# Kernel tuning notes

Hardware: AMD Instinct MI355X
Metric: run time of the kernel (lower is better)

Reference implementation:

```python
import jax, jax.numpy as jnp
import numpy as np

B, T, A, H, E = 512, 64, 32, 512, 32


def sinusoidal_pos_encoding(t, dim):
    # t: (B, T) float positions -> (B, T, dim)
    half = dim // 2
    freqs = jnp.exp(-jnp.log(10000.0) * jnp.arange(half, dtype=jnp.float32) / half)
    ang = t[..., None] * freqs  # (B, T, half)
    return jnp.concatenate([jnp.sin(ang), jnp.cos(ang)], axis=-1)


def cat_linear(x, W, b, cat_ids):
    # x: (B, T, Din); W: (E, Din, Dout); b: (E, Dout); cat_ids: (B,)
    Wg = W[cat_ids]            # (B, Din, Dout) gathered per-sample weights
    bg = b[cat_ids][:, None]   # (B, 1, Dout)
    return jnp.einsum('btd,bdh->bth', x, Wg) + bg


def swish(x):
    return x * jax.nn.sigmoid(x)


def setup_inputs() -> dict:
    key = jax.random.key(0)
    ks = jax.random.split(key, 10)
    s = lambda fan_in: 1.0 / np.sqrt(fan_in)
    return {
        'actions': jax.random.normal(ks[0], (B, T, A), dtype=jnp.float32),
        'timesteps': jax.random.uniform(ks[1], (B,), dtype=jnp.float32),
        'cat_ids': jax.random.randint(ks[2], (B,), 0, E),
        'W1': jax.random.normal(ks[3], (E, A, H), dtype=jnp.float32) * s(A),
        'b1': jnp.zeros((E, H), dtype=jnp.float32),
        'W2': jax.random.normal(ks[4], (E, 2 * H, H), dtype=jnp.float32) * s(2 * H),
        'b2': jnp.zeros((E, H), dtype=jnp.float32),
        'W3': jax.random.normal(ks[5], (E, H, H), dtype=jnp.float32) * s(H),
        'b3': jnp.zeros((E, H), dtype=jnp.float32),
    }


def reference(actions, timesteps, cat_ids, W1, b1, W2, b2, W3, b3):
    b, t, _ = actions.shape
    timesteps_bt = jnp.broadcast_to(timesteps[:, None], (b, t))
    a_emb = cat_linear(actions, W1, b1, cat_ids)              # (B, T, H)
    tau_emb = sinusoidal_pos_encoding(timesteps_bt, H).astype(a_emb.dtype)
    x = jnp.concatenate([a_emb, tau_emb], axis=-1)            # (B, T, 2H)
    x = swish(cat_linear(x, W2, b2, cat_ids))                 # (B, T, H)
    x = cat_linear(x, W3, b3, cat_ids)                        # (B, T, H)
    return x
```

## Files before the change

### kernel.cpp

```cpp
#include <hip/hip_runtime.h>
#include <hip/hip_bf16.h>

#define B_ 512
#define T_ 64
#define A_ 32
#define H_ 512
#define E_ 32
#define MAX_TASKS 272
#define CAP_ 168
#define GRID_ (8 * CAP_)

typedef unsigned short u16;
typedef unsigned int u32;
typedef __attribute__((ext_vector_type(8))) short short8;
typedef __attribute__((ext_vector_type(4))) float floatx4;

static __device__ __forceinline__ u16 f2bf(float f) {
    u32 u = __builtin_bit_cast(u32, f);
    u += 0x7fffu + ((u >> 16) & 1u);
    return (u16)(u >> 16);
}

static __device__ __forceinline__ void gl2lds16(const u16* g, u16* l) {
    __builtin_amdgcn_global_load_lds(
        (const __attribute__((address_space(1))) void*)g,
        (__attribute__((address_space(3))) void*)l, 16, 0, 0);
}

__global__ void group_kernel(const int* __restrict__ cat_ids,
                             int* __restrict__ sample_list,
                             int4* __restrict__ tasks,
                             int* __restrict__ itemlist) {
    __shared__ int cnt[E_], off[E_], cur[E_], toff[E_], jc[8];
    __shared__ int total, fb;
    int tid = threadIdx.x;
    if (tid < E_) { cnt[tid] = 0; cur[tid] = 0; }
    __syncthreads();
    int e = cat_ids[tid];
    atomicAdd(&cnt[e], 1);
    __syncthreads();
    if (tid == 0) {
        int run = 0, trun = 0;
        for (int i = 0; i < E_; i++) {
            off[i] = run;  run += cnt[i];
            toff[i] = trun; trun += (cnt[i] + 1) >> 1;
        }
        total = trun;
    }
    __syncthreads();
    if (tid < E_) {
        int c = cnt[tid], o = off[tid], to = toff[tid];
        for (int j = 0; j < c; j += 2)
            tasks[to++] = make_int4(tid, o + j, (c - j >= 2) ? 2 : 1, 0);
    }
    if (tid < 8) {
        int J = 0;
        for (int cc = 0; cc < 4; cc++) J += 4 * ((cnt[tid + 8 * cc] + 1) >> 1);
        jc[tid] = J;
    }
    __syncthreads();
    if (tid == 0) {
        int f = 0;
        for (int x = 0; x < 8; x++) if (jc[x] > CAP_) f = 1;
        fb = f;
    }
    __syncthreads();
    if (!fb) {
        if (tid < 8) {
            int j = 0;
            for (int cc = 0; cc < 4; cc++) {
                int ee = tid + 8 * cc;
                int nt = (cnt[ee] + 1) >> 1, t0 = toff[ee];
                for (int t = t0; t < t0 + nt; t++)
                    for (int nb = 0; nb < 4; nb++) {
                        itemlist[tid + 8 * j] = (t << 2) | nb;
                        j++;
                    }
            }
            for (; j < CAP_; j++) itemlist[tid + 8 * j] = -1;
        }
    } else {
        for (int f = tid; f < GRID_; f += 512)
            itemlist[f] = (f < 4 * total) ? f : -1;
    }
    int p = atomicAdd(&cur[e], 1);
    sample_list[off[e] + p] = tid;
}

__global__ __launch_bounds__(256) void embed_kernel(
        const float* __restrict__ actions, const float* __restrict__ timesteps,
        const int* __restrict__ cat_ids, const float* __restrict__ W1,
        const float* __restrict__ b1, u16* __restrict__ a_emb,
        u16* __restrict__ tau_emb) {
    int b = blockIdx.x;
    int tid = threadIdx.x;
    int e = cat_ids[b];
    float tval = timesteps[b];

    {
        float freq = expf(-9.210340371976184f * (float)tid * (1.0f / 256.0f));
        float ang = tval * freq;
        tau_emb[b * H_ + tid]       = f2bf(sinf(ang));
        tau_emb[b * H_ + 256 + tid] = f2bf(cosf(ang));
    }

    __shared__ float act[T_ * A_];
    const float* asrc = actions + (size_t)b * T_ * A_;
    for (int i = tid; i < T_ * A_; i += 256) act[i] = asrc[i];
    __syncthreads();

    const float* w1 = W1 + (size_t)e * A_ * H_;
    int n0 = tid, n1 = tid + 256;
    float wA[A_], wB[A_];
#pragma unroll
    for (int k = 0; k < A_; k++) {
        wA[k] = w1[k * H_ + n0];
        wB[k] = w1[k * H_ + n1];
    }
    float bA = b1[e * H_ + n0], bB = b1[e * H_ + n1];
    u16* orow = a_emb + (size_t)b * T_ * H_;
    for (int tt = 0; tt < T_; tt++) {
        float accA = bA, accB = bB;
#pragma unroll
        for (int k = 0; k < A_; k++) {
            float a = act[tt * A_ + k];
            accA = fmaf(a, wA[k], accA);
            accB = fmaf(a, wB[k], accB);
        }
        orow[tt * H_ + n0] = f2bf(accA);
        orow[tt * H_ + n1] = f2bf(accB);
    }
}

__global__ __launch_bounds__(256) void convert_transpose(
        const float* __restrict__ W, u16* __restrict__ Wt, int K) {
    int n = blockIdx.y * 256 + threadIdx.x;
    int k0 = blockIdx.x * 32;
    int e = blockIdx.z;
    const float* src = W + ((size_t)e * K + k0) * H_ + n;
    short8 out[4];
#pragma unroll
    for (int j = 0; j < 32; j++)
        out[j >> 3][j & 7] = (short)f2bf(src[(size_t)j * H_]);
    u16* dst = Wt + ((size_t)e * H_ + n) * K + k0;
#pragma unroll
    for (int c = 0; c < 4; c++) *(short8*)(dst + c * 8) = out[c];
}

template <int DIN, bool HAS_TAU, bool DO_SWISH, bool OUT_BF16>
__global__ __launch_bounds__(256, 4) void moe_gemm(
        const u16* __restrict__ xsrc, const u16* __restrict__ tau,
        const u16* __restrict__ Wt, const float* __restrict__ bias,
        const int* __restrict__ sample_list, const int4* __restrict__ tasks,
        const int* __restrict__ itemlist, void* __restrict__ outp) {
    int item = itemlist[blockIdx.x];
    if (item < 0) return;
    int4 task = tasks[item >> 2];
    int nb = item & 3;
    int ns = task.z;
    int e = task.x;
    int s0 = sample_list[task.y];
    int s1 = (ns > 1) ? sample_list[task.y + 1] : s0;
    int n0 = nb * 128;

    int tid = threadIdx.x;
    int lane = tid & 63, wv = tid >> 6;
    int wr = wv >> 1, wc = wv & 1;
    int quad = lane >> 4, c15 = lane & 15;
    int r8 = lane >> 3, cg = lane & 7;

    __shared__ __align__(16) u16 xs[128 * 64];
    __shared__ __align__(16) u16 wt[128 * 64];

    floatx4 acc[4][4];
    floatx4 zero4 = {0.f, 0.f, 0.f, 0.f};
#pragma unroll
    for (int i = 0; i < 4; i++)
#pragma unroll
        for (int j = 0; j < 4; j++) acc[i][j] = zero4;

    const u16* wbase = Wt + (size_t)(e * H_ + n0) * DIN;
    int kc_sw = (cg ^ r8) * 8;

    for (int k0 = 0; k0 < DIN; k0 += 64) {
        bool use_tau = HAS_TAU && (k0 >= 512);
#pragma unroll
        for (int h = 0; h < 4; h++) {
            int rbase = h * 32 + wv * 8;
            int row = rbase + r8;
            int s = (rbase < 64) ? s0 : s1;
            int t = row & 63;
            const u16* g = use_tau
                ? (tau + (size_t)s * H_ + (k0 - 512) + kc_sw)
                : (xsrc + ((size_t)s * T_ + t) * H_ + k0 + kc_sw);
            gl2lds16(g, &xs[rbase * 64]);
        }
#pragma unroll
        for (int h = 0; h < 4; h++) {
            int nbase = h * 32 + wv * 8;
            int nrow = nbase + r8;
            gl2lds16(wbase + (size_t)nrow * DIN + k0 + kc_sw, &wt[nbase * 64]);
        }
        __syncthreads();

#pragma unroll
        for (int kk = 0; kk < 2; kk++) {
            int c = kk * 4 + quad;
            short8 af[4], bfr[4];
#pragma unroll
            for (int i = 0; i < 4; i++) {
                int row = wr * 64 + i * 16 + c15;
                af[i] = *(const short8*)&xs[row * 64 + ((c ^ (row & 7)) * 8)];
                int nr = wc * 64 + i * 16 + c15;
                bfr[i] = *(const short8*)&wt[nr * 64 + ((c ^ (nr & 7)) * 8)];
            }
#pragma unroll
            for (int mt = 0; mt < 4; mt++)
#pragma unroll
                for (int nt = 0; nt < 4; nt++)
                    acc[mt][nt] = __builtin_amdgcn_mfma_f32_16x16x32_bf16(
                            af[mt], bfr[nt], acc[mt][nt], 0, 0, 0);
        }
        __syncthreads();
    }

    if (wr >= ns) return;
    int s = (wr == 0) ? s0 : s1;
    const float* bp = bias + (size_t)e * H_;
#pragma unroll
    for (int mt = 0; mt < 4; mt++) {
        int tb = mt * 16 + quad * 4;
#pragma unroll
        for (int nt = 0; nt < 4; nt++) {
            int col = n0 + wc * 64 + nt * 16 + c15;
            float bv = bp[col];
#pragma unroll
            for (int r = 0; r < 4; r++) {
                float v = acc[mt][nt][r] + bv;
                if (DO_SWISH) v = v / (1.0f + expf(-v));
                size_t oidx = ((size_t)s * T_ + tb + r) * H_ + col;
                if (OUT_BF16) ((u16*)outp)[oidx] = f2bf(v);
                else          ((float*)outp)[oidx] = v;
            }
        }
    }
}

extern "C" void kernel_launch(void* const* d_in, const int* in_sizes, int n_in,
                              void* d_out, int out_size, void* d_ws, size_t ws_size,
                              hipStream_t stream) {
    const float* actions   = (const float*)d_in[0];
    const float* timesteps = (const float*)d_in[1];
    const int*   cat_ids   = (const int*)d_in[2];
    const float* W1 = (const float*)d_in[3];
    const float* b1 = (const float*)d_in[4];
    const float* W2 = (const float*)d_in[5];
    const float* b2 = (const float*)d_in[6];
    const float* W3 = (const float*)d_in[7];
    const float* b3 = (const float*)d_in[8];

    char* ws = (char*)d_ws;
    u16* a_emb = (u16*)ws;
    u16* y     = (u16*)(ws + (size_t)32 * 1024 * 1024);
    u16* tau   = (u16*)(ws + (size_t)64 * 1024 * 1024);
    char* meta = ws + (size_t)64 * 1024 * 1024 + 512 * 1024;
    int*  sample_list = (int*)meta;
    int4* tasks       = (int4*)(meta + 8192);
    int*  itemlist    = (int*)(meta + 16384);
    u16* Wt2 = (u16*)d_out;
    u16* Wt3 = a_emb;

    hipLaunchKernelGGL(group_kernel, dim3(1), dim3(512), 0, stream,
                       cat_ids, sample_list, tasks, itemlist);
    hipLaunchKernelGGL(embed_kernel, dim3(512), dim3(256), 0, stream,
                       actions, timesteps, cat_ids, W1, b1, a_emb, tau);
    hipLaunchKernelGGL(convert_transpose, dim3(2 * H_ / 32, 2, E_), dim3(256),
                       0, stream, W2, Wt2, 2 * H_);
    hipLaunchKernelGGL((moe_gemm<2 * H_, true, true, true>), dim3(GRID_),
                       dim3(256), 0, stream,
                       a_emb, tau, Wt2, b2, sample_list, tasks, itemlist, (void*)y);
    hipLaunchKernelGGL(convert_transpose, dim3(H_ / 32, 2, E_), dim3(256),
                       0, stream, W3, Wt3, H_);
    hipLaunchKernelGGL((moe_gemm<H_, false, false, false>), dim3(GRID_),
                       dim3(256), 0, stream,
                       y, (const u16*)nullptr, Wt3, b3, sample_list, tasks,
                       itemlist, d_out);
}
```

Baseline: 301.7 us.

## Fold time-invariant tau half of layer-2 GEMM into per-sample bias; double-buffer LDS

The tau embedding is constant across the T dimension, so its product with the second half of W2 is computed once per sample in a new tau_bias_kernel, which writes a per-sample bias. The layer-2 GEMM then only runs over K=512 instead of 1024, and only the first half of W2 is converted and transposed. The moe_gemm K-loop also gains double-buffered LDS staging so the next tile's loads overlap the current MFMAs, with launch bounds lowered to 2 blocks per CU to fit the doubled LDS. The extra fp32 kernel adds a small launch and some redundant sin/cos evaluation, and reduced occupancy may offset some of the overlap.

```diff
diff --git a/kernel.cpp b/kernel.cpp
--- a/kernel.cpp
+++ b/kernel.cpp
@@ -9,6 +9,7 @@
 #define MAX_TASKS 272
 #define CAP_ 168
 #define GRID_ (8 * CAP_)
+#define SC 16
 
 typedef unsigned short u16;
 typedef unsigned int u32;
@@ -30,7 +31,9 @@
 __global__ void group_kernel(const int* __restrict__ cat_ids,
                              int* __restrict__ sample_list,
                              int4* __restrict__ tasks,
-                             int* __restrict__ itemlist) {
+                             int* __restrict__ itemlist,
+                             int* __restrict__ eoff_g,
+                             int* __restrict__ ecnt_g) {
     __shared__ int cnt[E_], off[E_], cur[E_], toff[E_], jc[8];
     __shared__ int total, fb;
     int tid = threadIdx.x;
@@ -50,6 +53,8 @@
     __syncthreads();
     if (tid < E_) {
         int c = cnt[tid], o = off[tid], to = toff[tid];
+        eoff_g[tid] = o;
+        ecnt_g[tid] = c;
         for (int j = 0; j < c; j += 2)
             tasks[to++] = make_int4(tid, o + j, (c - j >= 2) ? 2 : 1, 0);
     }
@@ -88,21 +93,12 @@
 }
 
 __global__ __launch_bounds__(256) void embed_kernel(
-        const float* __restrict__ actions, const float* __restrict__ timesteps,
-        const int* __restrict__ cat_ids, const float* __restrict__ W1,
-        const float* __restrict__ b1, u16* __restrict__ a_emb,
-        u16* __restrict__ tau_emb) {
+        const float* __restrict__ actions, const int* __restrict__ cat_ids,
+        const float* __restrict__ W1, const float* __restrict__ b1,
+        u16* __restrict__ a_emb) {
     int b = blockIdx.x;
     int tid = threadIdx.x;
     int e = cat_ids[b];
-    float tval = timesteps[b];
-
-    {
-        float freq = expf(-9.210340371976184f * (float)tid * (1.0f / 256.0f));
-        float ang = tval * freq;
-        tau_emb[b * H_ + tid]       = f2bf(sinf(ang));
-        tau_emb[b * H_ + 256 + tid] = f2bf(cosf(ang));
-    }
 
     __shared__ float act[T_ * A_];
     const float* asrc = actions + (size_t)b * T_ * A_;
@@ -133,24 +129,92 @@
 }
 
 __global__ __launch_bounds__(256) void convert_transpose(
-        const float* __restrict__ W, u16* __restrict__ Wt, int K) {
+        const float* __restrict__ W, u16* __restrict__ Wt, int srcK, int dstK) {
     int n = blockIdx.y * 256 + threadIdx.x;
     int k0 = blockIdx.x * 32;
     int e = blockIdx.z;
-    const float* src = W + ((size_t)e * K + k0) * H_ + n;
+    const float* src = W + ((size_t)e * srcK + k0) * H_ + n;
     short8 out[4];
 #pragma unroll
     for (int j = 0; j < 32; j++)
         out[j >> 3][j & 7] = (short)f2bf(src[(size_t)j * H_]);
-    u16* dst = Wt + ((size_t)e * H_ + n) * K + k0;
+    u16* dst = Wt + ((size_t)e * H_ + n) * dstK + k0;
 #pragma unroll
     for (int c = 0; c < 4; c++) *(short8*)(dst + c * 8) = out[c];
 }
 
-template <int DIN, bool HAS_TAU, bool DO_SWISH, bool OUT_BF16>
-__global__ __launch_bounds__(256, 4) void moe_gemm(
-        const u16* __restrict__ xsrc, const u16* __restrict__ tau,
-        const u16* __restrict__ Wt, const float* __restrict__ bias,
+__global__ __launch_bounds__(256) void tau_bias_kernel(
+        const float* __restrict__ W2, const float* __restrict__ b2,
+        const float* __restrict__ timesteps, const int* __restrict__ sample_list,
+        const int* __restrict__ eoff, const int* __restrict__ ecnt,
+        float* __restrict__ bias2s) {
+    int cc = blockIdx.x;
+    int e = blockIdx.y;
+    int cnt = ecnt[e], off = eoff[e];
+    if (cnt == 0) return;
+    int tid = threadIdx.x;
+    int kq = tid >> 6, lane = tid & 63;
+    int n = cc * 64 + lane;
+    __shared__ float tauS[SC][512];
+    __shared__ float pS[4][SC][64];
+    const float* wb = W2 + ((size_t)e * 1024 + 512) * H_;
+
+    for (int c0 = 0; c0 < cnt; c0 += SC) {
+        for (int i = tid; i < SC * 512; i += 256) {
+            int sl = i >> 9, k = i & 511;
+            float v = 0.f;
+            if (c0 + sl < cnt) {
+                int s = sample_list[off + c0 + sl];
+                float tval = timesteps[s];
+                int kk = k & 255;
+                float freq = expf(-9.210340371976184f * (float)kk * (1.0f / 256.0f));
+                float ang = tval * freq;
+                v = (k < 256) ? sinf(ang) : cosf(ang);
+            }
+            tauS[sl][k] = v;
+        }
+        __syncthreads();
+
+        float a[SC];
+#pragma unroll
+        for (int s = 0; s < SC; s++) a[s] = 0.f;
+        int kb = kq * 128;
+        for (int k = kb; k < kb + 128; k += 4) {
+            float w0 = wb[(size_t)k * H_ + n];
+            float w1 = wb[(size_t)(k + 1) * H_ + n];
+            float w2 = wb[(size_t)(k + 2) * H_ + n];
+            float w3 = wb[(size_t)(k + 3) * H_ + n];
+#pragma unroll
+            for (int s = 0; s < SC; s++) {
+                float4 t4 = *(const float4*)&tauS[s][k];
+                a[s] = fmaf(t4.x, w0, a[s]);
+                a[s] = fmaf(t4.y, w1, a[s]);
+                a[s] = fmaf(t4.z, w2, a[s]);
+                a[s] = fmaf(t4.w, w3, a[s]);
+            }
+        }
+#pragma unroll
+        for (int s = 0; s < SC; s++) pS[kq][s][lane] = a[s];
+        __syncthreads();
+
+        for (int o = tid; o < SC * 64; o += 256) {
+            int sl = o >> 6, ln = o & 63;
+            if (c0 + sl < cnt) {
+                float v = pS[0][sl][ln] + pS[1][sl][ln] +
+                          pS[2][sl][ln] + pS[3][sl][ln];
+                int s = sample_list[off + c0 + sl];
+                int col = cc * 64 + ln;
+                bias2s[(size_t)s * H_ + col] = v + b2[e * H_ + col];
+            }
+        }
+        __syncthreads();
+    }
+}
+
+template <int DIN, bool PSBIAS, bool DO_SWISH, bool OUT_BF16>
+__global__ __launch_bounds__(256, 2) void moe_gemm(
+        const u16* __restrict__ xsrc, const u16* __restrict__ Wt,
+        const float* __restrict__ bias,
         const int* __restrict__ sample_list, const int4* __restrict__ tasks,
         const int* __restrict__ itemlist, void* __restrict__ outp) {
     int item = itemlist[blockIdx.x];
@@ -169,8 +233,8 @@
     int quad = lane >> 4, c15 = lane & 15;
     int r8 = lane >> 3, cg = lane & 7;
 
-    __shared__ __align__(16) u16 xs[128 * 64];
-    __shared__ __align__(16) u16 wt[128 * 64];
+    __shared__ __align__(16) u16 xs[2][128 * 64];
+    __shared__ __align__(16) u16 wt[2][128 * 64];
 
     floatx4 acc[4][4];
     floatx4 zero4 = {0.f, 0.f, 0.f, 0.f};
@@ -182,27 +246,24 @@
     const u16* wbase = Wt + (size_t)(e * H_ + n0) * DIN;
     int kc_sw = (cg ^ r8) * 8;
 
-    for (int k0 = 0; k0 < DIN; k0 += 64) {
-        bool use_tau = HAS_TAU && (k0 >= 512);
+    auto stage = [&](int b, int k0) {
 #pragma unroll
         for (int h = 0; h < 4; h++) {
             int rbase = h * 32 + wv * 8;
-            int row = rbase + r8;
-            int s = (rbase < 64) ? s0 : s1;
-            int t = row & 63;
-            const u16* g = use_tau
-                ? (tau + (size_t)s * H_ + (k0 - 512) + kc_sw)
-                : (xsrc + ((size_t)s * T_ + t) * H_ + k0 + kc_sw);
-            gl2lds16(g, &xs[rbase * 64]);
+            int s = (h < 2) ? s0 : s1;
+            int t = (rbase + r8) & 63;
+            gl2lds16(xsrc + ((size_t)s * T_ + t) * H_ + k0 + kc_sw,
+                     &xs[b][rbase * 64]);
         }
 #pragma unroll
         for (int h = 0; h < 4; h++) {
             int nbase = h * 32 + wv * 8;
-            int nrow = nbase + r8;
-            gl2lds16(wbase + (size_t)nrow * DIN + k0 + kc_sw, &wt[nbase * 64]);
-        }
-        __syncthreads();
-
+            gl2lds16(wbase + (size_t)(nbase + r8) * DIN + k0 + kc_sw,
+                     &wt[b][nbase * 64]);
+        }
+    };
+
+    auto compute = [&](int b) {
 #pragma unroll
         for (int kk = 0; kk < 2; kk++) {
             int c = kk * 4 + quad;
@@ -210,9 +271,9 @@
 #pragma unroll
             for (int i = 0; i < 4; i++) {
                 int row = wr * 64 + i * 16 + c15;
-                af[i] = *(const short8*)&xs[row * 64 + ((c ^ (row & 7)) * 8)];
+                af[i] = *(const short8*)&xs[b][row * 64 + ((c ^ (row & 7)) * 8)];
                 int nr = wc * 64 + i * 16 + c15;
-                bfr[i] = *(const short8*)&wt[nr * 64 + ((c ^ (nr & 7)) * 8)];
+                bfr[i] = *(const short8*)&wt[b][nr * 64 + ((c ^ (nr & 7)) * 8)];
             }
 #pragma unroll
             for (int mt = 0; mt < 4; mt++)
@@ -221,12 +282,22 @@
                     acc[mt][nt] = __builtin_amdgcn_mfma_f32_16x16x32_bf16(
                             af[mt], bfr[nt], acc[mt][nt], 0, 0, 0);
         }
-        __syncthreads();
+    };
+
+    constexpr int KI = DIN / 64;
+    stage(0, 0);
+    __syncthreads();
+#pragma unroll
+    for (int t = 0; t < KI; ++t) {
+        if (t + 1 < KI) stage((t + 1) & 1, (t + 1) * 64);
+        compute(t & 1);
+        if (t + 1 < KI) __syncthreads();
     }
 
     if (wr >= ns) return;
     int s = (wr == 0) ? s0 : s1;
-    const float* bp = bias + (size_t)e * H_;
+    const float* bp = PSBIAS ? (bias + (size_t)s * H_)
+                             : (bias + (size_t)e * H_);
 #pragma unroll
     for (int mt = 0; mt < 4; mt++) {
         int tb = mt * 16 + quad * 4;
@@ -262,27 +333,31 @@
     char* ws = (char*)d_ws;
     u16* a_emb = (u16*)ws;
     u16* y     = (u16*)(ws + (size_t)32 * 1024 * 1024);
-    u16* tau   = (u16*)(ws + (size_t)64 * 1024 * 1024);
     char* meta = ws + (size_t)64 * 1024 * 1024 + 512 * 1024;
     int*  sample_list = (int*)meta;
     int4* tasks       = (int4*)(meta + 8192);
     int*  itemlist    = (int*)(meta + 16384);
-    u16* Wt2 = (u16*)d_out;
-    u16* Wt3 = a_emb;
+    int*  eoff        = (int*)(meta + 24576);
+    int*  ecnt        = (int*)(meta + 24576 + 128);
+    u16*  Wt2a   = (u16*)d_out;
+    float* bias2s = (float*)((char*)d_out + (size_t)48 * 1024 * 1024);
+    u16*  Wt3    = a_emb;
 
     hipLaunchKernelGGL(group_kernel, dim3(1), dim3(512), 0, stream,
-                       cat_ids, sample_list, tasks, itemlist);
+                       cat_ids, sample_list, tasks, itemlist, eoff, ecnt);
     hipLaunchKernelGGL(embed_kernel, dim3(512), dim3(256), 0, stream,
-                       actions, timesteps, cat_ids, W1, b1, a_emb, tau);
-    hipLaunchKernelGGL(convert_transpose, dim3(2 * H_ / 32, 2, E_), dim3(256),
-                       0, stream, W2, Wt2, 2 * H_);
-    hipLaunchKernelGGL((moe_gemm<2 * H_, true, true, true>), dim3(GRID_),
+                       actions, cat_ids, W1, b1, a_emb);
+    hipLaunchKernelGGL(convert_transpose, dim3(H_ / 32, 2, E_), dim3(256),
+                       0, stream, W2, Wt2a, 2 * H_, H_);
+    hipLaunchKernelGGL(tau_bias_kernel, dim3(8, E_), dim3(256), 0, stream,
+                       W2, b2, timesteps, sample_list, eoff, ecnt, bias2s);
+    hipLaunchKernelGGL((moe_gemm<H_, true, true, true>), dim3(GRID_),
                        dim3(256), 0, stream,
-                       a_emb, tau, Wt2, b2, sample_list, tasks, itemlist, (void*)y);
+                       a_emb, Wt2a, bias2s, sample_list, tasks, itemlist,
+                       (void*)y);
     hipLaunchKernelGGL(convert_transpose, dim3(H_ / 32, 2, E_), dim3(256),
-                       0, stream, W3, Wt3, H_);
+                       0, stream, W3, Wt3, H_, H_);
     hipLaunchKernelGGL((moe_gemm<H_, false, false, false>), dim3(GRID_),
                        dim3(256), 0, stream,
-                       y, (const u16*)nullptr, Wt3, b3, sample_list, tasks,
-                       itemlist, d_out);
-}
+                       y, Wt3, b3, sample_list, tasks, itemlist, d_out);
+}
```

Result: slower. 328.2 us (+8.8%).
